# Kernel optimization log

Measured on AMD Instinct MI355X. Metric: run time of the kernel, lower is better.

Reference implementation:

```python
import jax, jax.numpy as jnp
import numpy as np

B, H, W, C = 32, 56, 56, 256

def setup_inputs() -> dict:
    key = jax.random.key(0)
    k1, k2 = jax.random.split(key)
    x = jax.random.normal(k1, (B, H, W, C), dtype=jnp.float32)
    shift_map = jax.random.randint(k2, (B, H, W, 1), 0, C, dtype=jnp.int64)
    return {"x": x, "shift_map": shift_map}

def reference(x, shift_map):
    # Original TF op: left = x[..., m:], right = x[..., :m], out = concat(left, right)
    # i.e. a per-(b,h,w) circular LEFT roll of the channel axis by m = shift_map[...,0].
    c = x.shape[-1]
    m = shift_map.astype(jnp.int32)              # [B,H,W,1]
    idx = (jnp.arange(c, dtype=jnp.int32) + m) % c  # [B,H,W,C] gather indices
    return jnp.take_along_axis(x, idx, axis=-1)
```

## Files before the change

kernel.cpp:

```cpp
#include <hip/hip_runtime.h>


__global__ __launch_bounds__(256) void ChannelRoll_kernel(
    const float4* __restrict__ x4,
    const int*    __restrict__ shift,
    float4*       __restrict__ out4,
    int total4)
{
    int gid = blockIdx.x * blockDim.x + threadIdx.x;
    if (gid >= total4) return;

    int row  = gid >> 6;
    int lane = threadIdx.x & 63;

    float4 v = x4[gid];

    int m = shift[row] & 255;
    int q = m >> 2;
    int r = m & 3;

    float t0 = __shfl(v.x, (lane + q + (0 < r ? 1 : 0)) & 63, 64);
    float t1 = __shfl(v.y, (lane + q + (1 < r ? 1 : 0)) & 63, 64);
    float t2 = __shfl(v.z, (lane + q + (2 < r ? 1 : 0)) & 63, 64);
    float t3 = __shfl(v.w, (lane + q + (3 < r ? 1 : 0)) & 63, 64);

    float4 o;
    switch (r) {
        case 0:  o = make_float4(t0, t1, t2, t3); break;
        case 1:  o = make_float4(t1, t2, t3, t0); break;
        case 2:  o = make_float4(t2, t3, t0, t1); break;
        default: o = make_float4(t3, t0, t1, t2); break;
    }

    out4[gid] = o;
}

extern "C" void kernel_launch(void* const* d_in, const int* in_sizes, int n_in,
                              void* d_out, int out_size, void* d_ws, size_t ws_size,
                              hipStream_t stream)
{
    const float4* x4    = (const float4*)d_in[0];
    const int*    shift = (const int*)  d_in[1];
    float4*       out4  = (float4*)d_out;

    int total4 = in_sizes[0] >> 2;
    int blocks = (total4 + 255) / 256;

    hipLaunchKernelGGL(ChannelRoll_kernel, dim3(blocks), dim3(256), 0, stream,
                       x4, shift, out4, total4);
}
```

Before: 34.80 us.

## Use grid-stride loop with two rows per iteration and nontemporal loads/stores

Replaces the one-thread-per-float4 launch with a fixed 2048-block grid-stride loop in which each wave handles whole 256-channel rows. Each iteration processes two rows so more loads are in flight, and the accesses use nontemporal load/store builtins to avoid polluting cache with streamed data. This aims to cut block launch overhead and raise memory-level parallelism for a bandwidth-bound copy. A fixed grid size can underfill or unbalance the device, and nontemporal hints may not help on this hardware.

```diff
diff --git a/kernel.cpp b/kernel.cpp
--- a/kernel.cpp
+++ b/kernel.cpp
@@ -1,51 +1,69 @@
 #include <hip/hip_runtime.h>
 
 
-__global__ __launch_bounds__(256) void ChannelRoll_kernel(
-    const float4* __restrict__ x4,
-    const int*    __restrict__ shift,
-    float4*       __restrict__ out4,
-    int total4)
-{
-    int gid = blockIdx.x * blockDim.x + threadIdx.x;
-    if (gid >= total4) return;
+typedef float vfloat4 __attribute__((ext_vector_type(4)));
 
-    int row  = gid >> 6;
-    int lane = threadIdx.x & 63;
-
-    float4 v = x4[gid];
-
-    int m = shift[row] & 255;
+__device__ __forceinline__ vfloat4 roll_row(vfloat4 v, int m, int lane) {
     int q = m >> 2;
     int r = m & 3;
-
     float t0 = __shfl(v.x, (lane + q + (0 < r ? 1 : 0)) & 63, 64);
     float t1 = __shfl(v.y, (lane + q + (1 < r ? 1 : 0)) & 63, 64);
     float t2 = __shfl(v.z, (lane + q + (2 < r ? 1 : 0)) & 63, 64);
     float t3 = __shfl(v.w, (lane + q + (3 < r ? 1 : 0)) & 63, 64);
+    vfloat4 o;
+    switch (r) {
+        case 0:  o.x = t0; o.y = t1; o.z = t2; o.w = t3; break;
+        case 1:  o.x = t1; o.y = t2; o.z = t3; o.w = t0; break;
+        case 2:  o.x = t2; o.y = t3; o.z = t0; o.w = t1; break;
+        default: o.x = t3; o.y = t0; o.z = t1; o.w = t2; break;
+    }
+    return o;
+}
 
-    float4 o;
-    switch (r) {
-        case 0:  o = make_float4(t0, t1, t2, t3); break;
-        case 1:  o = make_float4(t1, t2, t3, t0); break;
-        case 2:  o = make_float4(t2, t3, t0, t1); break;
-        default: o = make_float4(t3, t0, t1, t2); break;
+__global__ __launch_bounds__(256) void ChannelRoll_kernel(
+    const vfloat4* __restrict__ x4,
+    const int*     __restrict__ shift,
+    vfloat4*       __restrict__ out4,
+    int nrows)
+{
+    int lane   = threadIdx.x & 63;
+    int wave   = (blockIdx.x * blockDim.x + threadIdx.x) >> 6;
+    int nwaves = (gridDim.x * blockDim.x) >> 6;
+
+    int row = wave;
+    for (; row + nwaves < nrows; row += 2 * nwaves) {
+        int rowB = row + nwaves;
+        int iA = (row  << 6) | lane;
+        int iB = (rowB << 6) | lane;
+        vfloat4 vA = __builtin_nontemporal_load(&x4[iA]);
+        vfloat4 vB = __builtin_nontemporal_load(&x4[iB]);
+        int mA = shift[row]  & 255;
+        int mB = shift[rowB] & 255;
+        vfloat4 oA = roll_row(vA, mA, lane);
+        vfloat4 oB = roll_row(vB, mB, lane);
+        __builtin_nontemporal_store(oA, &out4[iA]);
+        __builtin_nontemporal_store(oB, &out4[iB]);
     }
-
-    out4[gid] = o;
+    for (; row < nrows; row += nwaves) {
+        int i = (row << 6) | lane;
+        vfloat4 v = __builtin_nontemporal_load(&x4[i]);
+        int m = shift[row] & 255;
+        vfloat4 o = roll_row(v, m, lane);
+        __builtin_nontemporal_store(o, &out4[i]);
+    }
 }
 
 extern "C" void kernel_launch(void* const* d_in, const int* in_sizes, int n_in,
                               void* d_out, int out_size, void* d_ws, size_t ws_size,
                               hipStream_t stream)
 {
-    const float4* x4    = (const float4*)d_in[0];
-    const int*    shift = (const int*)  d_in[1];
-    float4*       out4  = (float4*)d_out;
+    const vfloat4* x4    = (const vfloat4*)d_in[0];
+    const int*     shift = (const int*)   d_in[1];
+    vfloat4*       out4  = (vfloat4*)d_out;
 
-    int total4 = in_sizes[0] >> 2;
-    int blocks = (total4 + 255) / 256;
+    int nrows  = in_sizes[0] >> 8;
+    int blocks = 2048;
 
     hipLaunchKernelGGL(ChannelRoll_kernel, dim3(blocks), dim3(256), 0, stream,
-                       x4, shift, out4, total4);
+                       x4, shift, out4, nrows);
 }
```

After: 39.43 us. 1.13x slower.
